# Kernel tuning notes

Measured on AMD Instinct MI355X. Metric: run time of the kernel, lower is better.

Reference implementation:

```python
import jax, jax.numpy as jnp
import numpy as np

DIM = 192
T, H, W = 6, 8, 8
NH = 6
HD = DIM // NH
HW = H * W
N = T * HW
SCALE = HD ** (-0.5)
B_ = 128


def _sine_pos_enc():
    # Faithful port of get_sine_position_encoding(window_size[1:], dim // 2).
    npf = DIM // 2
    ones = jnp.ones((1, H, W), jnp.float32)
    y_embed = jnp.cumsum(ones, axis=1)
    x_embed = jnp.cumsum(ones, axis=2)
    two_pi = 2.0 * np.pi
    y_embed = y_embed / (y_embed[:, -1:, :] + 1e-6) * two_pi
    x_embed = x_embed / (x_embed[:, :, -1:] + 1e-6) * two_pi
    dim_t = jnp.arange(npf, dtype=jnp.float32)
    dim_t = 10000.0 ** (2.0 * jnp.floor(dim_t / 2.0) / npf)
    pos_x = x_embed[:, :, :, None] / dim_t
    pos_y = y_embed[:, :, :, None] / dim_t
    pos_x = jnp.stack((jnp.sin(pos_x[..., 0::2]), jnp.cos(pos_x[..., 1::2])), axis=4).reshape(1, H, W, npf)
    pos_y = jnp.stack((jnp.sin(pos_y[..., 0::2]), jnp.cos(pos_y[..., 1::2])), axis=4).reshape(1, H, W, npf)
    pos = jnp.concatenate((pos_y, pos_x), axis=3)  # (1, H, W, DIM)
    return pos.reshape(1, HW, DIM)


def setup_inputs() -> dict:
    key = jax.random.key(0)
    ks = jax.random.split(key, 6)
    s = 0.02
    return {
        "x": jax.random.normal(ks[0], (B_, N, DIM), jnp.float32),
        "Wqkv": jax.random.normal(ks[1], (3 * DIM, DIM), jnp.float32) * s,
        "Wproj": jax.random.normal(ks[2], (DIM, 2 * DIM), jnp.float32) * s,
        "bproj": jnp.zeros((DIM,), jnp.float32),
        "gamma": jnp.ones((DIM,), jnp.float32),
        "beta": jnp.zeros((DIM,), jnp.float32),
        "W1": jax.random.normal(ks[3], (DIM, DIM), jnp.float32) * s,
        "b1": jnp.zeros((DIM,), jnp.float32),
        "W2": jax.random.normal(ks[4], (DIM, DIM), jnp.float32) * s,
        "b2": jnp.zeros((DIM,), jnp.float32),
    }


def reference(x, Wqkv, Wproj, bproj, gamma, beta, W1, b1, W2, b2):
    b = x.shape[0]
    pos = jnp.tile(_sine_pos_enc(), (1, T, 1))  # (1, N, DIM)
    qkv = (x + pos) @ Wqkv.T                      # (b, N, 3*DIM)
    qkv = qkv.reshape(b, N, 3, NH, HD).transpose(2, 0, 3, 1, 4)
    # temporal chunks: (b, NH, T, HW, HD)
    q = qkv[0].reshape(b, NH, T, HW, HD)
    k = qkv[1].reshape(b, NH, T, HW, HD)
    v = qkv[2].reshape(b, NH, T, HW, HD)
    # all T x T cross-frame attention pairs at once
    scores = jnp.einsum('bhind,bhjmd->ijbhnm', q * SCALE, k)  # (T,T,b,NH,HW,HW)
    attn = jax.nn.softmax(scores, axis=-1)
    o = jnp.einsum('ijbhnm,bhjmd->ijbnhd', attn, v).reshape(T, T, b, HW, DIM)
    # Faithful to torch's x.view(-1, B_, HW, C): raw reinterpretation, not a transpose.
    x_tmp = x.reshape(T, b, HW, DIM)
    xi = jnp.broadcast_to(x_tmp[:, None], (T, T, b, HW, DIM))
    x_att = jnp.concatenate((o, xi), axis=-1)     # (T,T,b,HW,2*DIM)
    y = x_att @ Wproj.T + bproj
    mu = jnp.mean(y, axis=-1, keepdims=True)
    var = jnp.var(y, axis=-1, keepdims=True)
    y = (y - mu) / jnp.sqrt(var + 1e-5) * gamma + beta
    y = jax.nn.gelu(y @ W1.T + b1, approximate=False) @ W2.T + b2
    acc = jnp.sum(y, axis=1)                       # sum over j -> (T,b,HW,DIM)
    x_out = x + acc.transpose(1, 0, 2, 3).reshape(b, N, DIM) / T
    return jnp.concatenate((x, x_out), axis=-1)
```

## Files before the change

kernel.cpp:

```cpp
#include <hip/hip_runtime.h>
#include <cmath>

#define TT   6
#define NB   128
#define DIM  192
#define SCALE 0.17677669529663687f

typedef __attribute__((ext_vector_type(8))) short v8s;
typedef __attribute__((ext_vector_type(4))) float v4f;

__device__ __forceinline__ short f2bf(float f) {
  union { float f; unsigned u; } v; v.f = f;
  unsigned r = v.u + 0x7fffu + ((v.u >> 16) & 1u);
  return (short)(r >> 16);
}

__global__ void prep_kernel(const float* __restrict__ Wqkv, const float* __restrict__ Wproj,
                            const float* __restrict__ W1, const float* __restrict__ W2,
                            short* __restrict__ dWqkv, short* __restrict__ dWproj,
                            short* __restrict__ dW1, short* __restrict__ dW2,
                            float* __restrict__ pos) {
  int idx = blockIdx.x * 256 + threadIdx.x;
  const float* src = nullptr; short* dst = nullptr; int off = 0;
  if (idx < 27648)      { src = Wqkv;  dst = dWqkv;  off = idx; }
  else if (idx < 46080) { src = Wproj; dst = dWproj; off = idx - 27648; }
  else if (idx < 55296) { src = W1;    dst = dW1;    off = idx - 46080; }
  else if (idx < 64512) { src = W2;    dst = dW2;    off = idx - 55296; }
  else if (idx < 67584) {
    int p0 = (idx - 64512) * 4;
    float4 r;
    float* rp = (float*)&r;
#pragma unroll
    for (int jj = 0; jj < 4; jj++) {
      int p = p0 + jj;
      int row = p / 192, c = p - row * 192;
      int e  = (c < 96) ? (row >> 3) : (row & 7);
      int cc = (c < 96) ? c : c - 96;
      int m = cc >> 1;
      float embed = (float)(e + 1) * (6.283185307179586f / 8.000001f);
      float dt = powf(10000.0f, (float)m * (1.0f / 48.0f));
      float ang = embed / dt;
      rp[jj] = (cc & 1) ? cosf(ang) : sinf(ang);
    }
    *(float4*)(pos + p0) = r;
    return;
  } else return;
  const float* s = src + off * 4;
  short4 r;
  r.x = f2bf(s[0]); r.y = f2bf(s[1]); r.z = f2bf(s[2]); r.w = f2bf(s[3]);
  *(short4*)(dst + off * 4) = r;
}

__global__ __launch_bounds__(256) void qkv_kernel(
    const float* __restrict__ x, const float* __restrict__ pos,
    const short* __restrict__ Wqkv_bf,
    short* __restrict__ Qb, short* __restrict__ Kb, short* __restrict__ Vtb) {
  __shared__ short XP[64 * 200];
  int bid = blockIdx.x;
  int xcd = bid & 7, idx = bid >> 3;
  int bq = idx / TT;
  int b = xcd * 16 + bq, t = idx - bq * TT;
  int tid = threadIdx.x, w = tid >> 6, lane = tid & 63;
  int l15 = lane & 15, quad = lane >> 4;
  const float* xrow = x + (size_t)(b * (TT * 64) + t * 64) * DIM;
  for (int c = tid; c < 64 * 24; c += 256) {
    int row = c / 24, col8 = (c - (c / 24) * 24) * 8;
    const float* xs = xrow + row * DIM + col8;
    const float* pp = pos + row * DIM + col8;
    v8s r8;
#pragma unroll
    for (int jj = 0; jj < 8; jj++) r8[jj] = f2bf(xs[jj] + pp[jj]);
    *(v8s*)(XP + row * 200 + col8) = r8;
  }
  __syncthreads();
  const v4f vzero = {0.f, 0.f, 0.f, 0.f};
  size_t obase = (size_t)(b * TT + t) * 64 * DIM;
#pragma unroll
  for (int cti = 0; cti < 9; cti++) {
    int r0 = w * 144 + cti * 16;
    v4f acc[4] = {vzero, vzero, vzero, vzero};
#pragma unroll
    for (int ks = 0; ks < 6; ks++) {
      v8s a = *(const v8s*)(Wqkv_bf + (size_t)(r0 + l15) * 192 + ks * 32 + quad * 8);
#pragma unroll
      for (int nt = 0; nt < 4; nt++) {
        v8s bb = *(const v8s*)(XP + (nt * 16 + l15) * 200 + ks * 32 + quad * 8);
        acc[nt] = __builtin_amdgcn_mfma_f32_16x16x32_bf16(a, bb, acc[nt], 0, 0, 0);
      }
    }
    int R = r0 + quad * 4;
#pragma unroll
    for (int nt = 0; nt < 4; nt++) {
      int hw = nt * 16 + l15;
      if (R < 192) {
        short4 s;
        s.x = f2bf(acc[nt][0] * SCALE); s.y = f2bf(acc[nt][1] * SCALE);
        s.z = f2bf(acc[nt][2] * SCALE); s.w = f2bf(acc[nt][3] * SCALE);
        *(short4*)(Qb + obase + (size_t)hw * 192 + R) = s;
      } else if (R < 384) {
        short4 s;
        s.x = f2bf(acc[nt][0]); s.y = f2bf(acc[nt][1]);
        s.z = f2bf(acc[nt][2]); s.w = f2bf(acc[nt][3]);
        *(short4*)(Kb + obase + (size_t)hw * 192 + (R - 192)) = s;
      } else {
#pragma unroll
        for (int r = 0; r < 4; r++)
          Vtb[obase + (size_t)(R - 384 + r) * 64 + hw] = f2bf(acc[nt][r]);
      }
    }
  }
}

__global__ __launch_bounds__(256, 4) void fused_all(
    const float* __restrict__ x,
    const short* __restrict__ Qb, const short* __restrict__ Kb,
    const short* __restrict__ Vtb,
    const short* __restrict__ Wproj_bf, const short* __restrict__ W1_bf,
    const short* __restrict__ W2_bf,
    const float* __restrict__ bproj, const float* __restrict__ gamma,
    const float* __restrict__ beta, const float* __restrict__ b1,
    const float* __restrict__ b2,
    float* __restrict__ out) {
  __shared__ short SP[32 * 200];
  __shared__ short HB[32 * 200];
  __shared__ float LNp[32][4][2];

  int bid = blockIdx.x;
  int xcd = bid & 7, idx = bid >> 3;
  int bq = idx / 12;
  int rem = idx - bq * 12;
  int i = rem >> 1, half = rem & 1;
  int b = xcd * 16 + bq;

  int tid = threadIdx.x, w = tid >> 6, lane = tid & 63;
  int l15 = lane & 15, quad = lane >> 4;
  int wc = w;
  int qt = w & 1, hg = w >> 1;
  int cb = wc * 48;
  const v4f vzero = {0.f, 0.f, 0.f, 0.f};

  const float* xi = x + (size_t)((i * NB + b) * 64 + half * 32) * DIM;
  for (int c = tid; c < 32 * 24; c += 256) {
    int row = c / 24, col8 = (c - (c / 24) * 24) * 8;
    const float* xs = xi + row * DIM + col8;
    v8s r8;
#pragma unroll
    for (int jj = 0; jj < 8; jj++) r8[jj] = f2bf(xs[jj]);
    *(v8s*)(SP + row * 200 + col8) = r8;
  }

  const short* Qi = Qb + (size_t)(b * TT + i) * 64 * DIM;
  v8s qa[3];
#pragma unroll
  for (int hh = 0; hh < 3; hh++)
    qa[hh] = *(const v8s*)(Qi + (size_t)(half * 32 + qt * 16 + l15) * 192 + (hg * 3 + hh) * 32 + quad * 8);

  v4f acc[3][2];
#pragma unroll
  for (int cti = 0; cti < 3; cti++)
#pragma unroll
    for (int nt = 0; nt < 2; nt++) acc[cti][nt] = vzero;

  __syncthreads();

  v4f y1x[3][2];
#pragma unroll
  for (int cti = 0; cti < 3; cti++)
#pragma unroll
    for (int nt = 0; nt < 2; nt++) y1x[cti][nt] = vzero;
#pragma unroll
  for (int ks = 0; ks < 6; ks++) {
    v8s bxi[2];
#pragma unroll
    for (int nt = 0; nt < 2; nt++)
      bxi[nt] = *(const v8s*)(SP + (nt * 16 + l15) * 200 + ks * 32 + quad * 8);
#pragma unroll
    for (int cti = 0; cti < 3; cti++) {
      v8s a = *(const v8s*)(Wproj_bf + (size_t)(cb + cti * 16 + l15) * 384 + 192 + ks * 32 + quad * 8);
#pragma unroll
      for (int nt = 0; nt < 2; nt++)
        y1x[cti][nt] = __builtin_amdgcn_mfma_f32_16x16x32_bf16(a, bxi[nt], y1x[cti][nt], 0, 0, 0);
    }
  }

  int srcA = l15 + ((lane & 16) << 1);
  int srcB = srcA + 16;
  bool hiq = (lane & 32) != 0;

  for (int j = 0; j < TT; j++) {
    __syncthreads();
    {
      const short* Kj = Kb + (size_t)(b * TT + j) * 64 * DIM;
      const short* Vj = Vtb + (size_t)(b * TT + j) * 64 * DIM;
#pragma unroll
      for (int hh = 0; hh < 3; hh++) {
        int h = hg * 3 + hh;
        v4f S[4];
#pragma unroll
        for (int cta = 0; cta < 4; cta++) {
          v8s akq = *(const v8s*)(Kj + (size_t)(cta * 16 + l15) * 192 + h * 32 + quad * 8);
          S[cta] = __builtin_amdgcn_mfma_f32_16x16x32_bf16(akq, qa[hh], vzero, 0, 0, 0);
        }
        float mx = -1e30f;
#pragma unroll
        for (int cta = 0; cta < 4; cta++)
#pragma unroll
          for (int r = 0; r < 4; r++) mx = fmaxf(mx, S[cta][r]);
        mx = fmaxf(mx, __shfl_xor(mx, 16, 64));
        mx = fmaxf(mx, __shfl_xor(mx, 32, 64));
        float sum = 0.f;
#pragma unroll
        for (int cta = 0; cta < 4; cta++)
#pragma unroll
          for (int r = 0; r < 4; r++) {
            float e = __expf(S[cta][r] - mx);
            S[cta][r] = e; sum += e;
          }
        sum += __shfl_xor(sum, 16, 64);
        sum += __shfl_xor(sum, 32, 64);
        float inv = 1.0f / sum;
        unsigned pk00, pk01, pk10, pk11, pk20, pk21, pk30, pk31;
        {
          float a0 = S[0][0] * inv, a1 = S[0][1] * inv, a2 = S[0][2] * inv, a3 = S[0][3] * inv;
          __asm__("v_cvt_pk_bf16_f32 %0, %1, %2" : "=v"(pk00) : "v"(a0), "v"(a1));
          __asm__("v_cvt_pk_bf16_f32 %0, %1, %2" : "=v"(pk01) : "v"(a2), "v"(a3));
          float b0 = S[1][0] * inv, b1_ = S[1][1] * inv, b2_ = S[1][2] * inv, b3 = S[1][3] * inv;
          __asm__("v_cvt_pk_bf16_f32 %0, %1, %2" : "=v"(pk10) : "v"(b0), "v"(b1_));
          __asm__("v_cvt_pk_bf16_f32 %0, %1, %2" : "=v"(pk11) : "v"(b2_), "v"(b3));
          float c0 = S[2][0] * inv, c1 = S[2][1] * inv, c2 = S[2][2] * inv, c3 = S[2][3] * inv;
          __asm__("v_cvt_pk_bf16_f32 %0, %1, %2" : "=v"(pk20) : "v"(c0), "v"(c1));
          __asm__("v_cvt_pk_bf16_f32 %0, %1, %2" : "=v"(pk21) : "v"(c2), "v"(c3));
          float d0 = S[3][0] * inv, d1 = S[3][1] * inv, d2 = S[3][2] * inv, d3 = S[3][3] * inv;
          __asm__("v_cvt_pk_bf16_f32 %0, %1, %2" : "=v"(pk30) : "v"(d0), "v"(d1));
          __asm__("v_cvt_pk_bf16_f32 %0, %1, %2" : "=v"(pk31) : "v"(d2), "v"(d3));
        }
        union { unsigned u[4]; v8s v; } B0, B1;
        {
          unsigned ta = (unsigned)__shfl((int)pk00, srcA), tb = (unsigned)__shfl((int)pk10, srcA);
          B0.u[0] = hiq ? tb : ta;
          ta = (unsigned)__shfl((int)pk01, srcA); tb = (unsigned)__shfl((int)pk11, srcA);
          B0.u[1] = hiq ? tb : ta;
          ta = (unsigned)__shfl((int)pk00, srcB); tb = (unsigned)__shfl((int)pk10, srcB);
          B0.u[2] = hiq ? tb : ta;
          ta = (unsigned)__shfl((int)pk01, srcB); tb = (unsigned)__shfl((int)pk11, srcB);
          B0.u[3] = hiq ? tb : ta;
          ta = (unsigned)__shfl((int)pk20, srcA); tb = (unsigned)__shfl((int)pk30, srcA);
          B1.u[0] = hiq ? tb : ta;
          ta = (unsigned)__shfl((int)pk21, srcA); tb = (unsigned)__shfl((int)pk31, srcA);
          B1.u[1] = hiq ? tb : ta;
          ta = (unsigned)__shfl((int)pk20, srcB); tb = (unsigned)__shfl((int)pk30, srcB);
          B1.u[2] = hiq ? tb : ta;
          ta = (unsigned)__shfl((int)pk21, srcB); tb = (unsigned)__shfl((int)pk31, srcB);
          B1.u[3] = hiq ? tb : ta;
        }
#pragma unroll
        for (int ct2 = 0; ct2 < 2; ct2++) {
          v8s av0 = *(const v8s*)(Vj + (size_t)(h * 32 + ct2 * 16 + l15) * 64 + quad * 8);
          v8s av1 = *(const v8s*)(Vj + (size_t)(h * 32 + ct2 * 16 + l15) * 64 + 32 + quad * 8);
          v4f o = __builtin_amdgcn_mfma_f32_16x16x32_bf16(av0, B0.v, vzero, 0, 0, 0);
          o = __builtin_amdgcn_mfma_f32_16x16x32_bf16(av1, B1.v, o, 0, 0, 0);
          short4 s;
          s.x = f2bf(o[0]); s.y = f2bf(o[1]); s.z = f2bf(o[2]); s.w = f2bf(o[3]);
          *(short4*)(&SP[(qt * 16 + l15) * 200 + h * 32 + ct2 * 16 + quad * 4]) = s;
        }
      }
    }
    __syncthreads();

    v4f y1[3][2];
#pragma unroll
    for (int cti = 0; cti < 3; cti++)
#pragma unroll
      for (int nt = 0; nt < 2; nt++) y1[cti][nt] = y1x[cti][nt];
#pragma unroll
    for (int ks = 0; ks < 6; ks++) {
      v8s bo[2];
#pragma unroll
      for (int nt = 0; nt < 2; nt++)
        bo[nt] = *(const v8s*)(SP + (nt * 16 + l15) * 200 + ks * 32 + quad * 8);
#pragma unroll
      for (int cti = 0; cti < 3; cti++) {
        v8s a = *(const v8s*)(Wproj_bf + (size_t)(cb + cti * 16 + l15) * 384 + ks * 32 + quad * 8);
#pragma unroll
        for (int nt = 0; nt < 2; nt++)
          y1[cti][nt] = __builtin_amdgcn_mfma_f32_16x16x32_bf16(a, bo[nt], y1[cti][nt], 0, 0, 0);
      }
    }
#pragma unroll
    for (int cti = 0; cti < 3; cti++) {
      float4 bp4 = *(const float4*)(bproj + cb + cti * 16 + quad * 4);
#pragma unroll
      for (int nt = 0; nt < 2; nt++) {
        y1[cti][nt][0] += bp4.x; y1[cti][nt][1] += bp4.y;
        y1[cti][nt][2] += bp4.z; y1[cti][nt][3] += bp4.w;
      }
    }
#pragma unroll
    for (int nt = 0; nt < 2; nt++) {
      float s1 = 0.f, s2 = 0.f;
#pragma unroll
      for (int cti = 0; cti < 3; cti++)
#pragma unroll
        for (int r = 0; r < 4; r++) { float v = y1[cti][nt][r]; s1 += v; s2 += v * v; }
      s1 += __shfl_xor(s1, 16, 64); s2 += __shfl_xor(s2, 16, 64);
      s1 += __shfl_xor(s1, 32, 64); s2 += __shfl_xor(s2, 32, 64);
      if (quad == 0) {
        LNp[nt * 16 + l15][wc][0] = s1;
        LNp[nt * 16 + l15][wc][1] = s2;
      }
    }
    __syncthreads();
    float mu[2], rs[2];
#pragma unroll
    for (int nt = 0; nt < 2; nt++) {
      int row = nt * 16 + l15;
      float s1 = 0.f, s2 = 0.f;
#pragma unroll
      for (int ww = 0; ww < 4; ww++) { s1 += LNp[row][ww][0]; s2 += LNp[row][ww][1]; }
      float m = s1 * (1.0f / 192.0f);
      mu[nt] = m; rs[nt] = rsqrtf(s2 * (1.0f / 192.0f) - m * m + 1e-5f);
    }
#pragma unroll
    for (int cti = 0; cti < 3; cti++) {
      float4 g4 = *(const float4*)(gamma + cb + cti * 16 + quad * 4);
      float4 be4 = *(const float4*)(beta + cb + cti * 16 + quad * 4);
#pragma unroll
      for (int nt = 0; nt < 2; nt++) {
        short4 s;
        s.x = f2bf((y1[cti][nt][0] - mu[nt]) * rs[nt] * g4.x + be4.x);
        s.y = f2bf((y1[cti][nt][1] - mu[nt]) * rs[nt] * g4.y + be4.y);
        s.z = f2bf((y1[cti][nt][2] - mu[nt]) * rs[nt] * g4.z + be4.z);
        s.w = f2bf((y1[cti][nt][3] - mu[nt]) * rs[nt] * g4.w + be4.w);
        *(short4*)(&SP[(nt * 16 + l15) * 200 + cb + cti * 16 + quad * 4]) = s;
      }
    }
    __syncthreads();

    v4f y2[3][2];
#pragma unroll
    for (int cti = 0; cti < 3; cti++)
#pragma unroll
      for (int nt = 0; nt < 2; nt++) y2[cti][nt] = vzero;
#pragma unroll
    for (int ks = 0; ks < 6; ks++) {
      v8s bh[2];
#pragma unroll
      for (int nt = 0; nt < 2; nt++)
        bh[nt] = *(const v8s*)(SP + (nt * 16 + l15) * 200 + ks * 32 + quad * 8);
#pragma unroll
      for (int cti = 0; cti < 3; cti++) {
        v8s a = *(const v8s*)(W1_bf + (size_t)(cb + cti * 16 + l15) * 192 + ks * 32 + quad * 8);
#pragma unroll
        for (int nt = 0; nt < 2; nt++)
          y2[cti][nt] = __builtin_amdgcn_mfma_f32_16x16x32_bf16(a, bh[nt], y2[cti][nt], 0, 0, 0);
      }
    }
#pragma unroll
    for (int cti = 0; cti < 3; cti++) {
      float4 b14 = *(const float4*)(b1 + cb + cti * 16 + quad * 4);
#pragma unroll
      for (int nt = 0; nt < 2; nt++) {
        float vv[4] = {y2[cti][nt][0] + b14.x, y2[cti][nt][1] + b14.y,
                       y2[cti][nt][2] + b14.z, y2[cti][nt][3] + b14.w};
        short sv[4];
#pragma unroll
        for (int r = 0; r < 4; r++) {
          float v = vv[r];
          float t = 0.79788456080286536f * (v + 0.044715f * v * v * v);
          float e = __expf(2.0f * t);
          float th = 1.0f - 2.0f / (e + 1.0f);
          sv[r] = f2bf(0.5f * v * (1.0f + th));
        }
        short4 s;
        s.x = sv[0]; s.y = sv[1]; s.z = sv[2]; s.w = sv[3];
        *(short4*)(&HB[(nt * 16 + l15) * 200 + cb + cti * 16 + quad * 4]) = s;
      }
    }
    __syncthreads();

#pragma unroll
    for (int ks = 0; ks < 6; ks++) {
      v8s bh[2];
#pragma unroll
      for (int nt = 0; nt < 2; nt++)
        bh[nt] = *(const v8s*)(HB + (nt * 16 + l15) * 200 + ks * 32 + quad * 8);
#pragma unroll
      for (int cti = 0; cti < 3; cti++) {
        v8s a = *(const v8s*)(W2_bf + (size_t)(cb + cti * 16 + l15) * 192 + ks * 32 + quad * 8);
#pragma unroll
        for (int nt = 0; nt < 2; nt++)
          acc[cti][nt] = __builtin_amdgcn_mfma_f32_16x16x32_bf16(a, bh[nt], acc[cti][nt], 0, 0, 0);
      }
    }
  }

  float* SPf = (float*)SP;
#pragma unroll
  for (int pass = 0; pass < 2; pass++) {
    __syncthreads();
#pragma unroll
    for (int cti = 0; cti < 3; cti++) {
      float4 o4;
      o4.x = acc[cti][pass][0] * (1.0f / 6.0f);
      o4.y = acc[cti][pass][1] * (1.0f / 6.0f);
      o4.z = acc[cti][pass][2] * (1.0f / 6.0f);
      o4.w = acc[cti][pass][3] * (1.0f / 6.0f);
      *(float4*)(&SPf[l15 * 196 + cb + cti * 16 + quad * 4]) = o4;
    }
    __syncthreads();
    for (int c = tid; c < 768; c += 256) {
      int r16 = c / 48, col4 = (c - r16 * 48) * 4;
      int row = half * 32 + pass * 16 + r16;
      size_t nrow = (size_t)b * 384 + (size_t)i * 64 + row;
      float4 xv = *(const float4*)(x + nrow * DIM + col4);
      float4 b24 = *(const float4*)(b2 + col4);
      float4 av = *(const float4*)(&SPf[r16 * 196 + col4]);
      float4 o4;
      o4.x = xv.x + av.x + b24.x;
      o4.y = xv.y + av.y + b24.y;
      o4.z = xv.z + av.z + b24.z;
      o4.w = xv.w + av.w + b24.w;
      *(float4*)(out + nrow * 384 + col4) = xv;
      *(float4*)(out + nrow * 384 + 192 + col4) = o4;
    }
  }
}

extern "C" void kernel_launch(void* const* d_in, const int* in_sizes, int n_in,
                              void* d_out, int out_size, void* d_ws, size_t ws_size,
                              hipStream_t stream) {
  (void)in_sizes; (void)n_in; (void)out_size; (void)ws_size;
  const float* x     = (const float*)d_in[0];
  const float* Wqkv  = (const float*)d_in[1];
  const float* Wproj = (const float*)d_in[2];
  const float* bproj = (const float*)d_in[3];
  const float* gamma = (const float*)d_in[4];
  const float* beta  = (const float*)d_in[5];
  const float* W1    = (const float*)d_in[6];
  const float* b1    = (const float*)d_in[7];
  const float* W2    = (const float*)d_in[8];
  const float* b2    = (const float*)d_in[9];
  float* out = (float*)d_out;

  short* Wqkv_bf  = (short*)d_ws;
  short* Wproj_bf = Wqkv_bf + 110592;
  short* W1_bf    = Wproj_bf + 73728;
  short* W2_bf    = W1_bf + 36864;
  float* pos_f    = (float*)(W2_bf + 36864);
  short* Qb       = (short*)(pos_f + 12288);
  short* Kb       = Qb + 9437184;
  short* Vtb      = Kb + 9437184;

  prep_kernel<<<dim3(264), dim3(256), 0, stream>>>(
      Wqkv, Wproj, W1, W2, Wqkv_bf, Wproj_bf, W1_bf, W2_bf, pos_f);
  qkv_kernel<<<dim3(TT * NB), dim3(256), 0, stream>>>(x, pos_f, Wqkv_bf, Qb, Kb, Vtb);
  fused_all<<<dim3(TT * NB * 2), dim3(256), 0, stream>>>(
      x, Qb, Kb, Vtb, Wproj_bf, W1_bf, W2_bf, bproj, gamma, beta, b1, b2, out);
}
```

Measured before the change: 561.8 us.

## Process two key frames per iteration to reuse weight loads and halve barriers

The j loop over key frames is unrolled by two, with separate shared buffers for each frame's attention output, LayerNorm input and GELU hidden state. Each weight fragment loaded from global memory (Wproj, W1, W2) now feeds MFMAs for both frames, and the number of block barriers per frame is halved. The cost is double the LDS footprint (about 51KB per block, which may cut the 4-blocks-per-CU occupancy) and higher register pressure from the duplicated accumulators, which could cause spills under the launch bounds.

```diff
diff --git a/kernel.cpp b/kernel.cpp
--- a/kernel.cpp
+++ b/kernel.cpp
@@ -111,6 +111,45 @@
   }
 }
 
+__device__ __forceinline__ void ptrans(const v4f S[4], float inv,
+                                       int srcA, int srcB, bool hiq,
+                                       v8s& B0v, v8s& B1v) {
+  unsigned pk00, pk01, pk10, pk11, pk20, pk21, pk30, pk31;
+  {
+    float a0 = S[0][0] * inv, a1 = S[0][1] * inv, a2 = S[0][2] * inv, a3 = S[0][3] * inv;
+    __asm__("v_cvt_pk_bf16_f32 %0, %1, %2" : "=v"(pk00) : "v"(a0), "v"(a1));
+    __asm__("v_cvt_pk_bf16_f32 %0, %1, %2" : "=v"(pk01) : "v"(a2), "v"(a3));
+    float b0 = S[1][0] * inv, b1_ = S[1][1] * inv, b2_ = S[1][2] * inv, b3 = S[1][3] * inv;
+    __asm__("v_cvt_pk_bf16_f32 %0, %1, %2" : "=v"(pk10) : "v"(b0), "v"(b1_));
+    __asm__("v_cvt_pk_bf16_f32 %0, %1, %2" : "=v"(pk11) : "v"(b2_), "v"(b3));
+    float c0 = S[2][0] * inv, c1 = S[2][1] * inv, c2 = S[2][2] * inv, c3 = S[2][3] * inv;
+    __asm__("v_cvt_pk_bf16_f32 %0, %1, %2" : "=v"(pk20) : "v"(c0), "v"(c1));
+    __asm__("v_cvt_pk_bf16_f32 %0, %1, %2" : "=v"(pk21) : "v"(c2), "v"(c3));
+    float d0 = S[3][0] * inv, d1 = S[3][1] * inv, d2 = S[3][2] * inv, d3 = S[3][3] * inv;
+    __asm__("v_cvt_pk_bf16_f32 %0, %1, %2" : "=v"(pk30) : "v"(d0), "v"(d1));
+    __asm__("v_cvt_pk_bf16_f32 %0, %1, %2" : "=v"(pk31) : "v"(d2), "v"(d3));
+  }
+  union { unsigned u[4]; v8s v; } B0, B1;
+  unsigned ta, tb;
+  ta = (unsigned)__shfl((int)pk00, srcA); tb = (unsigned)__shfl((int)pk10, srcA);
+  B0.u[0] = hiq ? tb : ta;
+  ta = (unsigned)__shfl((int)pk01, srcA); tb = (unsigned)__shfl((int)pk11, srcA);
+  B0.u[1] = hiq ? tb : ta;
+  ta = (unsigned)__shfl((int)pk00, srcB); tb = (unsigned)__shfl((int)pk10, srcB);
+  B0.u[2] = hiq ? tb : ta;
+  ta = (unsigned)__shfl((int)pk01, srcB); tb = (unsigned)__shfl((int)pk11, srcB);
+  B0.u[3] = hiq ? tb : ta;
+  ta = (unsigned)__shfl((int)pk20, srcA); tb = (unsigned)__shfl((int)pk30, srcA);
+  B1.u[0] = hiq ? tb : ta;
+  ta = (unsigned)__shfl((int)pk21, srcA); tb = (unsigned)__shfl((int)pk31, srcA);
+  B1.u[1] = hiq ? tb : ta;
+  ta = (unsigned)__shfl((int)pk20, srcB); tb = (unsigned)__shfl((int)pk30, srcB);
+  B1.u[2] = hiq ? tb : ta;
+  ta = (unsigned)__shfl((int)pk21, srcB); tb = (unsigned)__shfl((int)pk31, srcB);
+  B1.u[3] = hiq ? tb : ta;
+  B0v = B0.v; B1v = B1.v;
+}
+
 __global__ __launch_bounds__(256, 4) void fused_all(
     const float* __restrict__ x,
     const short* __restrict__ Qb, const short* __restrict__ Kb,
@@ -121,9 +160,11 @@
     const float* __restrict__ beta, const float* __restrict__ b1,
     const float* __restrict__ b2,
     float* __restrict__ out) {
-  __shared__ short SP[32 * 200];
-  __shared__ short HB[32 * 200];
-  __shared__ float LNp[32][4][2];
+  __shared__ short SPa[32 * 200];
+  __shared__ short SPb[32 * 200];
+  __shared__ short HBa[32 * 200];
+  __shared__ short HBb[32 * 200];
+  __shared__ float LNp[2][32][4][2];
 
   int bid = blockIdx.x;
   int xcd = bid & 7, idx = bid >> 3;
@@ -146,7 +187,7 @@
     v8s r8;
 #pragma unroll
     for (int jj = 0; jj < 8; jj++) r8[jj] = f2bf(xs[jj]);
-    *(v8s*)(SP + row * 200 + col8) = r8;
+    *(v8s*)(SPa + row * 200 + col8) = r8;
   }
 
   const short* Qi = Qb + (size_t)(b * TT + i) * 64 * DIM;
@@ -173,7 +214,7 @@
     v8s bxi[2];
 #pragma unroll
     for (int nt = 0; nt < 2; nt++)
-      bxi[nt] = *(const v8s*)(SP + (nt * 16 + l15) * 200 + ks * 32 + quad * 8);
+      bxi[nt] = *(const v8s*)(SPa + (nt * 16 + l15) * 200 + ks * 32 + quad * 8);
 #pragma unroll
     for (int cti = 0; cti < 3; cti++) {
       v8s a = *(const v8s*)(Wproj_bf + (size_t)(cb + cti * 16 + l15) * 384 + 192 + ks * 32 + quad * 8);
@@ -187,103 +228,90 @@
   int srcB = srcA + 16;
   bool hiq = (lane & 32) != 0;
 
-  for (int j = 0; j < TT; j++) {
+  for (int j = 0; j < TT; j += 2) {
     __syncthreads();
     {
-      const short* Kj = Kb + (size_t)(b * TT + j) * 64 * DIM;
-      const short* Vj = Vtb + (size_t)(b * TT + j) * 64 * DIM;
+      const short* Kja = Kb + (size_t)(b * TT + j) * 64 * DIM;
+      const short* Vja = Vtb + (size_t)(b * TT + j) * 64 * DIM;
+      const short* Kjb = Kja + 64 * DIM;
+      const short* Vjb = Vja + 64 * DIM;
 #pragma unroll
       for (int hh = 0; hh < 3; hh++) {
         int h = hg * 3 + hh;
-        v4f S[4];
+        v4f Sa[4], Sb[4];
 #pragma unroll
         for (int cta = 0; cta < 4; cta++) {
-          v8s akq = *(const v8s*)(Kj + (size_t)(cta * 16 + l15) * 192 + h * 32 + quad * 8);
-          S[cta] = __builtin_amdgcn_mfma_f32_16x16x32_bf16(akq, qa[hh], vzero, 0, 0, 0);
-        }
-        float mx = -1e30f;
+          v8s ka = *(const v8s*)(Kja + (size_t)(cta * 16 + l15) * 192 + h * 32 + quad * 8);
+          Sa[cta] = __builtin_amdgcn_mfma_f32_16x16x32_bf16(ka, qa[hh], vzero, 0, 0, 0);
+        }
+#pragma unroll
+        for (int cta = 0; cta < 4; cta++) {
+          v8s kb = *(const v8s*)(Kjb + (size_t)(cta * 16 + l15) * 192 + h * 32 + quad * 8);
+          Sb[cta] = __builtin_amdgcn_mfma_f32_16x16x32_bf16(kb, qa[hh], vzero, 0, 0, 0);
+        }
+        float mxa = -1e30f, mxb = -1e30f;
 #pragma unroll
         for (int cta = 0; cta < 4; cta++)
 #pragma unroll
-          for (int r = 0; r < 4; r++) mx = fmaxf(mx, S[cta][r]);
-        mx = fmaxf(mx, __shfl_xor(mx, 16, 64));
-        mx = fmaxf(mx, __shfl_xor(mx, 32, 64));
-        float sum = 0.f;
+          for (int r = 0; r < 4; r++) { mxa = fmaxf(mxa, Sa[cta][r]); mxb = fmaxf(mxb, Sb[cta][r]); }
+        mxa = fmaxf(mxa, __shfl_xor(mxa, 16, 64)); mxb = fmaxf(mxb, __shfl_xor(mxb, 16, 64));
+        mxa = fmaxf(mxa, __shfl_xor(mxa, 32, 64)); mxb = fmaxf(mxb, __shfl_xor(mxb, 32, 64));
+        float suma = 0.f, sumb = 0.f;
 #pragma unroll
         for (int cta = 0; cta < 4; cta++)
 #pragma unroll
           for (int r = 0; r < 4; r++) {
-            float e = __expf(S[cta][r] - mx);
-            S[cta][r] = e; sum += e;
+            float ea = __expf(Sa[cta][r] - mxa); Sa[cta][r] = ea; suma += ea;
+            float eb = __expf(Sb[cta][r] - mxb); Sb[cta][r] = eb; sumb += eb;
           }
-        sum += __shfl_xor(sum, 16, 64);
-        sum += __shfl_xor(sum, 32, 64);
-        float inv = 1.0f / sum;
-        unsigned pk00, pk01, pk10, pk11, pk20, pk21, pk30, pk31;
-        {
-          float a0 = S[0][0] * inv, a1 = S[0][1] * inv, a2 = S[0][2] * inv, a3 = S[0][3] * inv;
-          __asm__("v_cvt_pk_bf16_f32 %0, %1, %2" : "=v"(pk00) : "v"(a0), "v"(a1));
-          __asm__("v_cvt_pk_bf16_f32 %0, %1, %2" : "=v"(pk01) : "v"(a2), "v"(a3));
-          float b0 = S[1][0] * inv, b1_ = S[1][1] * inv, b2_ = S[1][2] * inv, b3 = S[1][3] * inv;
-          __asm__("v_cvt_pk_bf16_f32 %0, %1, %2" : "=v"(pk10) : "v"(b0), "v"(b1_));
-          __asm__("v_cvt_pk_bf16_f32 %0, %1, %2" : "=v"(pk11) : "v"(b2_), "v"(b3));
-          float c0 = S[2][0] * inv, c1 = S[2][1] * inv, c2 = S[2][2] * inv, c3 = S[2][3] * inv;
-          __asm__("v_cvt_pk_bf16_f32 %0, %1, %2" : "=v"(pk20) : "v"(c0), "v"(c1));
-          __asm__("v_cvt_pk_bf16_f32 %0, %1, %2" : "=v"(pk21) : "v"(c2), "v"(c3));
-          float d0 = S[3][0] * inv, d1 = S[3][1] * inv, d2 = S[3][2] * inv, d3 = S[3][3] * inv;
-          __asm__("v_cvt_pk_bf16_f32 %0, %1, %2" : "=v"(pk30) : "v"(d0), "v"(d1));
-          __asm__("v_cvt_pk_bf16_f32 %0, %1, %2" : "=v"(pk31) : "v"(d2), "v"(d3));
-        }
-        union { unsigned u[4]; v8s v; } B0, B1;
-        {
-          unsigned ta = (unsigned)__shfl((int)pk00, srcA), tb = (unsigned)__shfl((int)pk10, srcA);
-          B0.u[0] = hiq ? tb : ta;
-          ta = (unsigned)__shfl((int)pk01, srcA); tb = (unsigned)__shfl((int)pk11, srcA);
-          B0.u[1] = hiq ? tb : ta;
-          ta = (unsigned)__shfl((int)pk00, srcB); tb = (unsigned)__shfl((int)pk10, srcB);
-          B0.u[2] = hiq ? tb : ta;
-          ta = (unsigned)__shfl((int)pk01, srcB); tb = (unsigned)__shfl((int)pk11, srcB);
-          B0.u[3] = hiq ? tb : ta;
-          ta = (unsigned)__shfl((int)pk20, srcA); tb = (unsigned)__shfl((int)pk30, srcA);
-          B1.u[0] = hiq ? tb : ta;
-          ta = (unsigned)__shfl((int)pk21, srcA); tb = (unsigned)__shfl((int)pk31, srcA);
-          B1.u[1] = hiq ? tb : ta;
-          ta = (unsigned)__shfl((int)pk20, srcB); tb = (unsigned)__shfl((int)pk30, srcB);
-          B1.u[2] = hiq ? tb : ta;
-          ta = (unsigned)__shfl((int)pk21, srcB); tb = (unsigned)__shfl((int)pk31, srcB);
-          B1.u[3] = hiq ? tb : ta;
-        }
+        suma += __shfl_xor(suma, 16, 64); sumb += __shfl_xor(sumb, 16, 64);
+        suma += __shfl_xor(suma, 32, 64); sumb += __shfl_xor(sumb, 32, 64);
+        float inva = 1.0f / suma, invb = 1.0f / sumb;
+        v8s B0a, B1a, B0b, B1b;
+        ptrans(Sa, inva, srcA, srcB, hiq, B0a, B1a);
+        ptrans(Sb, invb, srcA, srcB, hiq, B0b, B1b);
 #pragma unroll
         for (int ct2 = 0; ct2 < 2; ct2++) {
-          v8s av0 = *(const v8s*)(Vj + (size_t)(h * 32 + ct2 * 16 + l15) * 64 + quad * 8);
-          v8s av1 = *(const v8s*)(Vj + (size_t)(h * 32 + ct2 * 16 + l15) * 64 + 32 + quad * 8);
-          v4f o = __builtin_amdgcn_mfma_f32_16x16x32_bf16(av0, B0.v, vzero, 0, 0, 0);
-          o = __builtin_amdgcn_mfma_f32_16x16x32_bf16(av1, B1.v, o, 0, 0, 0);
-          short4 s;
-          s.x = f2bf(o[0]); s.y = f2bf(o[1]); s.z = f2bf(o[2]); s.w = f2bf(o[3]);
-          *(short4*)(&SP[(qt * 16 + l15) * 200 + h * 32 + ct2 * 16 + quad * 4]) = s;
-        }
-      }
-    }
-    __syncthreads();
-
-    v4f y1[3][2];
+          v8s av0a = *(const v8s*)(Vja + (size_t)(h * 32 + ct2 * 16 + l15) * 64 + quad * 8);
+          v8s av1a = *(const v8s*)(Vja + (size_t)(h * 32 + ct2 * 16 + l15) * 64 + 32 + quad * 8);
+          v4f oa = __builtin_amdgcn_mfma_f32_16x16x32_bf16(av0a, B0a, vzero, 0, 0, 0);
+          oa = __builtin_amdgcn_mfma_f32_16x16x32_bf16(av1a, B1a, oa, 0, 0, 0);
+          short4 sa;
+          sa.x = f2bf(oa[0]); sa.y = f2bf(oa[1]); sa.z = f2bf(oa[2]); sa.w = f2bf(oa[3]);
+          *(short4*)(&SPa[(qt * 16 + l15) * 200 + h * 32 + ct2 * 16 + quad * 4]) = sa;
+          v8s av0b = *(const v8s*)(Vjb + (size_t)(h * 32 + ct2 * 16 + l15) * 64 + quad * 8);
+          v8s av1b = *(const v8s*)(Vjb + (size_t)(h * 32 + ct2 * 16 + l15) * 64 + 32 + quad * 8);
+          v4f ob = __builtin_amdgcn_mfma_f32_16x16x32_bf16(av0b, B0b, vzero, 0, 0, 0);
+          ob = __builtin_amdgcn_mfma_f32_16x16x32_bf16(av1b, B1b, ob, 0, 0, 0);
+          short4 sb;
+          sb.x = f2bf(ob[0]); sb.y = f2bf(ob[1]); sb.z = f2bf(ob[2]); sb.w = f2bf(ob[3]);
+          *(short4*)(&SPb[(qt * 16 + l15) * 200 + h * 32 + ct2 * 16 + quad * 4]) = sb;
+        }
+      }
+    }
+    __syncthreads();
+
+    v4f y1a[3][2], y1b[3][2];
 #pragma unroll
     for (int cti = 0; cti < 3; cti++)
 #pragma unroll
-      for (int nt = 0; nt < 2; nt++) y1[cti][nt] = y1x[cti][nt];
+      for (int nt = 0; nt < 2; nt++) { y1a[cti][nt] = y1x[cti][nt]; y1b[cti][nt] = y1x[cti][nt]; }
 #pragma unroll
     for (int ks = 0; ks < 6; ks++) {
-      v8s bo[2];
-#pragma unroll
-      for (int nt = 0; nt < 2; nt++)
-        bo[nt] = *(const v8s*)(SP + (nt * 16 + l15) * 200 + ks * 32 + quad * 8);
+      v8s boa[2], bob[2];
+#pragma unroll
+      for (int nt = 0; nt < 2; nt++) {
+        boa[nt] = *(const v8s*)(SPa + (nt * 16 + l15) * 200 + ks * 32 + quad * 8);
+        bob[nt] = *(const v8s*)(SPb + (nt * 16 + l15) * 200 + ks * 32 + quad * 8);
+      }
 #pragma unroll
       for (int cti = 0; cti < 3; cti++) {
         v8s a = *(const v8s*)(Wproj_bf + (size_t)(cb + cti * 16 + l15) * 384 + ks * 32 + quad * 8);
 #pragma unroll
-        for (int nt = 0; nt < 2; nt++)
-          y1[cti][nt] = __builtin_amdgcn_mfma_f32_16x16x32_bf16(a, bo[nt], y1[cti][nt], 0, 0, 0);
+        for (int nt = 0; nt < 2; nt++) {
+          y1a[cti][nt] = __builtin_amdgcn_mfma_f32_16x16x32_bf16(a, boa[nt], y1a[cti][nt], 0, 0, 0);
+          y1b[cti][nt] = __builtin_amdgcn_mfma_f32_16x16x32_bf16(a, bob[nt], y1b[cti][nt], 0, 0, 0);
+        }
       }
     }
 #pragma unroll
@@ -291,34 +319,45 @@
       float4 bp4 = *(const float4*)(bproj + cb + cti * 16 + quad * 4);
 #pragma unroll
       for (int nt = 0; nt < 2; nt++) {
-        y1[cti][nt][0] += bp4.x; y1[cti][nt][1] += bp4.y;
-        y1[cti][nt][2] += bp4.z; y1[cti][nt][3] += bp4.w;
+        y1a[cti][nt][0] += bp4.x; y1a[cti][nt][1] += bp4.y;
+        y1a[cti][nt][2] += bp4.z; y1a[cti][nt][3] += bp4.w;
+        y1b[cti][nt][0] += bp4.x; y1b[cti][nt][1] += bp4.y;
+        y1b[cti][nt][2] += bp4.z; y1b[cti][nt][3] += bp4.w;
       }
     }
 #pragma unroll
     for (int nt = 0; nt < 2; nt++) {
-      float s1 = 0.f, s2 = 0.f;
+      float s1a = 0.f, s2a = 0.f, s1b = 0.f, s2b = 0.f;
 #pragma unroll
       for (int cti = 0; cti < 3; cti++)
 #pragma unroll
-        for (int r = 0; r < 4; r++) { float v = y1[cti][nt][r]; s1 += v; s2 += v * v; }
-      s1 += __shfl_xor(s1, 16, 64); s2 += __shfl_xor(s2, 16, 64);
-      s1 += __shfl_xor(s1, 32, 64); s2 += __shfl_xor(s2, 32, 64);
+        for (int r = 0; r < 4; r++) {
+          float va = y1a[cti][nt][r]; s1a += va; s2a += va * va;
+          float vb = y1b[cti][nt][r]; s1b += vb; s2b += vb * vb;
+        }
+      s1a += __shfl_xor(s1a, 16, 64); s2a += __shfl_xor(s2a, 16, 64);
+      s1a += __shfl_xor(s1a, 32, 64); s2a += __shfl_xor(s2a, 32, 64);
+      s1b += __shfl_xor(s1b, 16, 64); s2b += __shfl_xor(s2b, 16, 64);
+      s1b += __shfl_xor(s1b, 32, 64); s2b += __shfl_xor(s2b, 32, 64);
       if (quad == 0) {
-        LNp[nt * 16 + l15][wc][0] = s1;
-        LNp[nt * 16 + l15][wc][1] = s2;
-      }
-    }
-    __syncthreads();
-    float mu[2], rs[2];
+        LNp[0][nt * 16 + l15][wc][0] = s1a; LNp[0][nt * 16 + l15][wc][1] = s2a;
+        LNp[1][nt * 16 + l15][wc][0] = s1b; LNp[1][nt * 16 + l15][wc][1] = s2b;
+      }
+    }
+    __syncthreads();
+    float mua[2], rsa[2], mub[2], rsb[2];
 #pragma unroll
     for (int nt = 0; nt < 2; nt++) {
       int row = nt * 16 + l15;
-      float s1 = 0.f, s2 = 0.f;
-#pragma unroll
-      for (int ww = 0; ww < 4; ww++) { s1 += LNp[row][ww][0]; s2 += LNp[row][ww][1]; }
-      float m = s1 * (1.0f / 192.0f);
-      mu[nt] = m; rs[nt] = rsqrtf(s2 * (1.0f / 192.0f) - m * m + 1e-5f);
+      float s1a = 0.f, s2a = 0.f, s1b = 0.f, s2b = 0.f;
+#pragma unroll
+      for (int ww = 0; ww < 4; ww++) {
+        s1a += LNp[0][row][ww][0]; s2a += LNp[0][row][ww][1];
+        s1b += LNp[1][row][ww][0]; s2b += LNp[1][row][ww][1];
+      }
+      float ma = s1a * (1.0f / 192.0f), mb = s1b * (1.0f / 192.0f);
+      mua[nt] = ma; rsa[nt] = rsqrtf(s2a * (1.0f / 192.0f) - ma * ma + 1e-5f);
+      mub[nt] = mb; rsb[nt] = rsqrtf(s2b * (1.0f / 192.0f) - mb * mb + 1e-5f);
     }
 #pragma unroll
     for (int cti = 0; cti < 3; cti++) {
@@ -326,33 +365,42 @@
       float4 be4 = *(const float4*)(beta + cb + cti * 16 + quad * 4);
 #pragma unroll
       for (int nt = 0; nt < 2; nt++) {
-        short4 s;
-        s.x = f2bf((y1[cti][nt][0] - mu[nt]) * rs[nt] * g4.x + be4.x);
-        s.y = f2bf((y1[cti][nt][1] - mu[nt]) * rs[nt] * g4.y + be4.y);
-        s.z = f2bf((y1[cti][nt][2] - mu[nt]) * rs[nt] * g4.z + be4.z);
-        s.w = f2bf((y1[cti][nt][3] - mu[nt]) * rs[nt] * g4.w + be4.w);
-        *(short4*)(&SP[(nt * 16 + l15) * 200 + cb + cti * 16 + quad * 4]) = s;
-      }
-    }
-    __syncthreads();
-
-    v4f y2[3][2];
+        short4 sa, sb;
+        sa.x = f2bf((y1a[cti][nt][0] - mua[nt]) * rsa[nt] * g4.x + be4.x);
+        sa.y = f2bf((y1a[cti][nt][1] - mua[nt]) * rsa[nt] * g4.y + be4.y);
+        sa.z = f2bf((y1a[cti][nt][2] - mua[nt]) * rsa[nt] * g4.z + be4.z);
+        sa.w = f2bf((y1a[cti][nt][3] - mua[nt]) * rsa[nt] * g4.w + be4.w);
+        *(short4*)(&SPa[(nt * 16 + l15) * 200 + cb + cti * 16 + quad * 4]) = sa;
+        sb.x = f2bf((y1b[cti][nt][0] - mub[nt]) * rsb[nt] * g4.x + be4.x);
+        sb.y = f2bf((y1b[cti][nt][1] - mub[nt]) * rsb[nt] * g4.y + be4.y);
+        sb.z = f2bf((y1b[cti][nt][2] - mub[nt]) * rsb[nt] * g4.z + be4.z);
+        sb.w = f2bf((y1b[cti][nt][3] - mub[nt]) * rsb[nt] * g4.w + be4.w);
+        *(short4*)(&SPb[(nt * 16 + l15) * 200 + cb + cti * 16 + quad * 4]) = sb;
+      }
+    }
+    __syncthreads();
+
+    v4f y2a[3][2], y2b[3][2];
 #pragma unroll
     for (int cti = 0; cti < 3; cti++)
 #pragma unroll
-      for (int nt = 0; nt < 2; nt++) y2[cti][nt] = vzero;
+      for (int nt = 0; nt < 2; nt++) { y2a[cti][nt] = vzero; y2b[cti][nt] = vzero; }
 #pragma unroll
     for (int ks = 0; ks < 6; ks++) {
-      v8s bh[2];
-#pragma unroll
-      for (int nt = 0; nt < 2; nt++)
-        bh[nt] = *(const v8s*)(SP + (nt * 16 + l15) * 200 + ks * 32 + quad * 8);
+      v8s bha[2], bhb[2];
+#pragma unroll
+      for (int nt = 0; nt < 2; nt++) {
+        bha[nt] = *(const v8s*)(SPa + (nt * 16 + l15) * 200 + ks * 32 + quad * 8);
+        bhb[nt] = *(const v8s*)(SPb + (nt * 16 + l15) * 200 + ks * 32 + quad * 8);
+      }
 #pragma unroll
       for (int cti = 0; cti < 3; cti++) {
         v8s a = *(const v8s*)(W1_bf + (size_t)(cb + cti * 16 + l15) * 192 + ks * 32 + quad * 8);
 #pragma unroll
-        for (int nt = 0; nt < 2; nt++)
-          y2[cti][nt] = __builtin_amdgcn_mfma_f32_16x16x32_bf16(a, bh[nt], y2[cti][nt], 0, 0, 0);
+        for (int nt = 0; nt < 2; nt++) {
+          y2a[cti][nt] = __builtin_amdgcn_mfma_f32_16x16x32_bf16(a, bha[nt], y2a[cti][nt], 0, 0, 0);
+          y2b[cti][nt] = __builtin_amdgcn_mfma_f32_16x16x32_bf16(a, bhb[nt], y2b[cti][nt], 0, 0, 0);
+        }
       }
     }
 #pragma unroll
@@ -360,41 +408,49 @@
       float4 b14 = *(const float4*)(b1 + cb + cti * 16 + quad * 4);
 #pragma unroll
       for (int nt = 0; nt < 2; nt++) {
-        float vv[4] = {y2[cti][nt][0] + b14.x, y2[cti][nt][1] + b14.y,
-                       y2[cti][nt][2] + b14.z, y2[cti][nt][3] + b14.w};
-        short sv[4];
+        short sva[4], svb[4];
 #pragma unroll
         for (int r = 0; r < 4; r++) {
-          float v = vv[r];
-          float t = 0.79788456080286536f * (v + 0.044715f * v * v * v);
-          float e = __expf(2.0f * t);
-          float th = 1.0f - 2.0f / (e + 1.0f);
-          sv[r] = f2bf(0.5f * v * (1.0f + th));
-        }
-        short4 s;
-        s.x = sv[0]; s.y = sv[1]; s.z = sv[2]; s.w = sv[3];
-        *(short4*)(&HB[(nt * 16 + l15) * 200 + cb + cti * 16 + quad * 4]) = s;
+          float bb = (r == 0) ? b14.x : (r == 1) ? b14.y : (r == 2) ? b14.z : b14.w;
+          float va = y2a[cti][nt][r] + bb;
+          float ta = 0.79788456080286536f * (va + 0.044715f * va * va * va);
+          float ea = __expf(2.0f * ta);
+          sva[r] = f2bf(0.5f * va * (1.0f + (1.0f - 2.0f / (ea + 1.0f))));
+          float vb = y2b[cti][nt][r] + bb;
+          float tb = 0.79788456080286536f * (vb + 0.044715f * vb * vb * vb);
+          float eb = __expf(2.0f * tb);
+          svb[r] = f2bf(0.5f * vb * (1.0f + (1.0f - 2.0f / (eb + 1.0f))));
+        }
+        short4 sa, sb;
+        sa.x = sva[0]; sa.y = sva[1]; sa.z = sva[2]; sa.w = sva[3];
+        sb.x = svb[0]; sb.y = svb[1]; sb.z = svb[2]; sb.w = svb[3];
+        *(short4*)(&HBa[(nt * 16 + l15) * 200 + cb + cti * 16 + quad * 4]) = sa;
+        *(short4*)(&HBb[(nt * 16 + l15) * 200 + cb + cti * 16 + quad * 4]) = sb;
       }
     }
     __syncthreads();
 
 #pragma unroll
     for (int ks = 0; ks < 6; ks++) {
-      v8s bh[2];
-#pragma unroll
-      for (int nt = 0; nt < 2; nt++)
-        bh[nt] = *(const v8s*)(HB + (nt * 16 + l15) * 200 + ks * 32 + quad * 8);
+      v8s bha[2], bhb[2];
+#pragma unroll
+      for (int nt = 0; nt < 2; nt++) {
+        bha[nt] = *(const v8s*)(HBa + (nt * 16 + l15) * 200 + ks * 32 + quad * 8);
+        bhb[nt] = *(const v8s*)(HBb + (nt * 16 + l15) * 200 + ks * 32 + quad * 8);
+      }
 #pragma unroll
       for (int cti = 0; cti < 3; cti++) {
         v8s a = *(const v8s*)(W2_bf + (size_t)(cb + cti * 16 + l15) * 192 + ks * 32 + quad * 8);
 #pragma unroll
-        for (int nt = 0; nt < 2; nt++)
-          acc[cti][nt] = __builtin_amdgcn_mfma_f32_16x16x32_bf16(a, bh[nt], acc[cti][nt], 0, 0, 0);
-      }
-    }
-  }
-
-  float* SPf = (float*)SP;
+        for (int nt = 0; nt < 2; nt++) {
+          acc[cti][nt] = __builtin_amdgcn_mfma_f32_16x16x32_bf16(a, bha[nt], acc[cti][nt], 0, 0, 0);
+          acc[cti][nt] = __builtin_amdgcn_mfma_f32_16x16x32_bf16(a, bhb[nt], acc[cti][nt], 0, 0, 0);
+        }
+      }
+    }
+  }
+
+  float* SPf = (float*)SPa;
 #pragma unroll
   for (int pass = 0; pass < 2; pass++) {
     __syncthreads();
```

Result: slower. 633.1 us (+12.7%).
